# Optimization experiments

Measured on AMD Instinct MI355X. Metric: run time of the kernel, lower is better.

## Reference

```python
import jax, jax.numpy as jnp
import numpy as np

B, T, F, H = 256, 256, 128, 512


def setup_inputs() -> dict:
    key = jax.random.key(0)
    ks = jax.random.split(key, 16)
    values = jax.random.normal(ks[0], (B, T, F), dtype=jnp.float32)
    masks = (jax.random.uniform(ks[1], (B, T, F)) < 0.7).astype(jnp.float32)
    deltas = jax.random.uniform(ks[2], (B, T, F), dtype=jnp.float32) * 5.0
    empirical_mean = jax.random.normal(ks[3], (F,), dtype=jnp.float32)
    X_filledLOCF = jax.random.normal(ks[4], (B, T, F), dtype=jnp.float32)
    # TemporalDecay params: temp_decay_x is diag (F->F, diagonal weight), temp_decay_h is full (F->H)
    sF = 1.0 / np.sqrt(F)
    wx_diag = jax.random.uniform(ks[5], (F,), minval=-sF, maxval=sF, dtype=jnp.float32)
    bx = jax.random.uniform(ks[6], (F,), minval=-sF, maxval=sF, dtype=jnp.float32)
    Wh = jax.random.uniform(ks[7], (H, F), minval=-sF, maxval=sF, dtype=jnp.float32)
    bh = jax.random.uniform(ks[8], (H,), minval=-sF, maxval=sF, dtype=jnp.float32)
    # GRUCell params, torch layout: weight_ih [3H, 2F+H], weight_hh [3H, H], gate order r,z,n
    sH = 1.0 / np.sqrt(H)
    in_dim = 2 * F + H
    W_ih = jax.random.uniform(ks[9], (3 * H, in_dim), minval=-sH, maxval=sH, dtype=jnp.float32)
    W_hh = jax.random.uniform(ks[10], (3 * H, H), minval=-sH, maxval=sH, dtype=jnp.float32)
    b_ih = jax.random.uniform(ks[11], (3 * H,), minval=-sH, maxval=sH, dtype=jnp.float32)
    b_hh = jax.random.uniform(ks[12], (3 * H,), minval=-sH, maxval=sH, dtype=jnp.float32)
    return {"values": values, "masks": masks, "deltas": deltas,
            "empirical_mean": empirical_mean, "X_filledLOCF": X_filledLOCF,
            "wx_diag": wx_diag, "bx": bx, "Wh": Wh, "bh": bh,
            "W_ih": W_ih, "W_hh": W_hh, "b_ih": b_ih, "b_hh": b_hh}


def _grud_scan(values, masks, deltas, empirical_mean, X_filledLOCF,
               wx_diag, bx, Wh, bh, W_ih, W_hh, b_ih, b_hh):
    Hd = Wh.shape[0]
    h0 = jnp.zeros((values.shape[0], Hd), dtype=values.dtype)

    def step(h, xt):
        x, m, d, x_locf = xt  # each [B, F]
        gamma_h = jnp.exp(-jax.nn.relu(d @ Wh.T + bh))          # [B, H]
        gamma_x = jnp.exp(-jax.nn.relu(d * wx_diag + bx))       # [B, F] (diag TemporalDecay)
        h = h * gamma_h
        x_h = gamma_x * x_locf + (1.0 - gamma_x) * empirical_mean
        x_rep = m * x + (1.0 - m) * x_h
        inp = jnp.concatenate([x_rep, h, m], axis=1)            # [B, 2F+H]
        gi = inp @ W_ih.T + b_ih                                # [B, 3H]
        gh = h @ W_hh.T + b_hh                                  # [B, 3H]
        i_r, i_z, i_n = jnp.split(gi, 3, axis=1)
        h_r, h_z, h_n = jnp.split(gh, 3, axis=1)
        r = jax.nn.sigmoid(i_r + h_r)
        z = jax.nn.sigmoid(i_z + h_z)
        n = jnp.tanh(i_n + r * h_n)
        h_new = (1.0 - z) * n + z * h
        return h_new, h_new

    # time-major for scan: [T, B, F]
    xs = (values.transpose(1, 0, 2), masks.transpose(1, 0, 2),
          deltas.transpose(1, 0, 2), X_filledLOCF.transpose(1, 0, 2))
    h_last, hs = jax.lax.scan(step, h0, xs)
    return hs.transpose(1, 0, 2), h_last  # [B, T, H], [B, H]


def reference(values, masks, deltas, empirical_mean, X_filledLOCF,
              wx_diag, bx, Wh, bh, W_ih, W_hh, b_ih, b_hh):
    return _grud_scan(values, masks, deltas, empirical_mean, X_filledLOCF,
                      wx_diag, bx, Wh, bh, W_ih, W_hh, b_ih, b_hh)
```

## Files before the change

### kernel.cpp

```cpp
#include <hip/hip_runtime.h>
#include <math.h>

#define Bb 256
#define Tt 256
#define Ff 128
#define Hh 512
#define KTOT 768
#define NC 2048

typedef unsigned short u16;
typedef unsigned int   u32;
typedef unsigned long long u64;
typedef __attribute__((ext_vector_type(8))) short s8v;
typedef __attribute__((ext_vector_type(4))) float f4v;

#define OFF_GAMMA 0ull
#define OFF_XREP  (OFF_GAMMA + 67108864ull)
#define OFF_MBF   (OFF_XREP  + 16777216ull)
#define OFF_WFRAG (OFF_MBF   + 16777216ull)
#define OFF_BIASC (OFF_WFRAG + 3145728ull)
#define OFF_BAR   (OFF_BIASC + 8192ull)

__device__ __forceinline__ u16 f2b(float x) {
    u32 u = __float_as_uint(x);
    return (u16)((u + 0x7FFFu + ((u >> 16) & 1u)) >> 16);
}
__device__ __forceinline__ float b2f(u16 b) {
    return __uint_as_float(((u32)b) << 16);
}

__global__ __launch_bounds__(256) void k_zero(int* p, int n) {
    int i = blockIdx.x * 256 + threadIdx.x;
    if (i < n) p[i] = 0;
}

__device__ __forceinline__ float xrep_one(float x, float m, float d, float l,
                                          float w, float bb, float em) {
    float gx = expf(-fmaxf(d * w + bb, 0.f));
    float xh = gx * l + (1.f - gx) * em;
    return m * x + (1.f - m) * xh;
}

__global__ __launch_bounds__(256) void k_prep(const float* __restrict__ values,
                                              const float* __restrict__ masks,
                                              const float* __restrict__ deltas,
                                              const float* __restrict__ locf,
                                              const float* __restrict__ emean,
                                              const float* __restrict__ wx,
                                              const float* __restrict__ bxp,
                                              u16* __restrict__ xrep,
                                              u16* __restrict__ mbf) {
    int idx = blockIdx.x * 256 + threadIdx.x;
    int e = idx * 4;
    int f = e & 127;
    float4 xv = *(const float4*)&values[e];
    float4 mv = *(const float4*)&masks[e];
    float4 dv = *(const float4*)&deltas[e];
    float4 lv = *(const float4*)&locf[e];
    float4 wv = *(const float4*)&wx[f];
    float4 bv = *(const float4*)&bxp[f];
    float4 ev = *(const float4*)&emean[f];
    u16 o[4], mo[4];
    o[0] = f2b(xrep_one(xv.x, mv.x, dv.x, lv.x, wv.x, bv.x, ev.x));
    o[1] = f2b(xrep_one(xv.y, mv.y, dv.y, lv.y, wv.y, bv.y, ev.y));
    o[2] = f2b(xrep_one(xv.z, mv.z, dv.z, lv.z, wv.z, bv.z, ev.z));
    o[3] = f2b(xrep_one(xv.w, mv.w, dv.w, lv.w, wv.w, bv.w, ev.w));
    mo[0] = f2b(mv.x); mo[1] = f2b(mv.y); mo[2] = f2b(mv.z); mo[3] = f2b(mv.w);
    *(uint2*)&xrep[e] = *(uint2*)o;
    *(uint2*)&mbf[e]  = *(uint2*)mo;
}

__global__ __launch_bounds__(256) void k_wcomb(const float* __restrict__ W_ih,
                                               const float* __restrict__ W_hh,
                                               const float* __restrict__ b_ih,
                                               const float* __restrict__ b_hh,
                                               u16* __restrict__ wfrag,
                                               float* __restrict__ biasc) {
    int G = blockIdx.x * 256 + threadIdx.x;
    int lane = G & 63;
    int q = G >> 6;
    int ki = q % 24; q /= 24;
    int nt = q & 1;  q >>= 1;
    int wv = q & 3;  q >>= 2;
    int bx = q;
    int c = bx * 128 + wv * 32 + nt * 16 + (lane & 15);
    int kbase = ki * 32 + (lane >> 4) * 8;
    int g = c & 3, jH = c >> 2;
    u16 o[8];
#pragma unroll
    for (int j = 0; j < 8; ++j) {
        int k = kbase + j;
        float w;
        if (g < 3) {
            w = W_ih[(size_t)(g * Hh + jH) * KTOT + k];
            if (g < 2 && k >= Ff && k < Ff + Hh) w += W_hh[(size_t)(g * Hh + jH) * Hh + (k - Ff)];
        } else {
            w = (k >= Ff && k < Ff + Hh) ? W_hh[(size_t)(2 * Hh + jH) * Hh + (k - Ff)] : 0.f;
        }
        o[j] = f2b(w);
    }
    *(uint4*)&wfrag[(size_t)G * 8] = *(uint4*)o;
    if (ki == 0 && (lane >> 4) == 0) {
        float bv;
        if (g == 0)      bv = b_ih[jH] + b_hh[jH];
        else if (g == 1) bv = b_ih[Hh + jH] + b_hh[Hh + jH];
        else if (g == 2) bv = b_ih[2 * Hh + jH];
        else             bv = b_hh[2 * Hh + jH];
        biasc[c] = bv;
    }
}

__global__ __launch_bounds__(256) void k_gamma(const float* __restrict__ deltas,
                                               const float* __restrict__ Wh,
                                               const float* __restrict__ bh,
                                               u16* __restrict__ gamma) {
    __shared__ float A_s[64][68];
    __shared__ float B_s[64][68];
    int tid = threadIdx.x;
    int tx = tid & 15, ty = tid >> 4;
    int bt0 = blockIdx.x * 64;
    int c0  = blockIdx.y * 64;

    float acc[4][4];
#pragma unroll
    for (int i = 0; i < 4; ++i)
#pragma unroll
        for (int j = 0; j < 4; ++j) acc[i][j] = 0.f;

    for (int kc = 0; kc < 2; ++kc) {
#pragma unroll
        for (int s = 0; s < 4; ++s) {
            int v = tid + s * 256;
            int row = v >> 4, c4 = v & 15, kk = c4 * 4;
            int bt = bt0 + row;
            int b = bt & 255, tt = bt >> 8;
            float4 a = *(const float4*)&deltas[b * (Tt * Ff) + tt * Ff + kc * 64 + kk];
            *(float4*)&A_s[row][kk] = a;
        }
#pragma unroll
        for (int s = 0; s < 4; ++s) {
            int v = tid + s * 256;
            int col = v >> 4, c4 = v & 15, kk = c4 * 4;
            float4 w = *(const float4*)&Wh[(c0 + col) * Ff + kc * 64 + kk];
            *(float4*)&B_s[col][kk] = w;
        }
        __syncthreads();
#pragma unroll
        for (int kk = 0; kk < 64; kk += 4) {
            float4 a[4], b[4];
#pragma unroll
            for (int i = 0; i < 4; ++i) a[i] = *(const float4*)&A_s[4 * ty + i][kk];
#pragma unroll
            for (int j = 0; j < 4; ++j) b[j] = *(const float4*)&B_s[4 * tx + j][kk];
#pragma unroll
            for (int i = 0; i < 4; ++i)
#pragma unroll
                for (int j = 0; j < 4; ++j) {
                    acc[i][j] += a[i].x * b[j].x;
                    acc[i][j] += a[i].y * b[j].y;
                    acc[i][j] += a[i].z * b[j].z;
                    acc[i][j] += a[i].w * b[j].w;
                }
        }
        __syncthreads();
    }
#pragma unroll
    for (int i = 0; i < 4; ++i) {
        int bt = bt0 + 4 * ty + i;
        u16 o[4];
#pragma unroll
        for (int j = 0; j < 4; ++j) {
            int col = c0 + 4 * tx + j;
            float x = acc[i][j] + bh[col];
            o[j] = f2b(expf(-fmaxf(x, 0.f)));
        }
        *(uint2*)&gamma[(size_t)bt * Hh + c0 + 4 * tx] = *(uint2*)o;
    }
}

__global__ __launch_bounds__(256, 1) void k_scan(const u16* __restrict__ xrep,
                                                 const u16* __restrict__ mbf,
                                                 const u16* __restrict__ gamma,
                                                 const u16* __restrict__ wfrag,
                                                 const float* __restrict__ biasc,
                                                 int* __restrict__ bar,
                                                 float* __restrict__ hs,
                                                 float* __restrict__ hlast) {
    __shared__ u16  A_s[24 * 64 * 8];
    __shared__ float E_s[16][132];

    int tid = threadIdx.x;
    int lane = tid & 63, w = tid >> 6;

    int L = blockIdx.x + 16 * blockIdx.y;
    int by = (L & 7) + 8 * (L >> 7);
    int bx = (L >> 3) & 15;
    int r0 = by * 16;

    uint4 Bf[2][24];
    const uint4* wf4 = (const uint4*)wfrag;
#pragma unroll
    for (int nt = 0; nt < 2; ++nt)
#pragma unroll
        for (int ki = 0; ki < 24; ++ki)
            Bf[nt][ki] = wf4[(size_t)((((bx * 4 + w) * 2 + nt) * 24 + ki) * 64 + lane)];

    int srow = lane & 15;
    int koff = (lane >> 4) * 8;

    int bl = tid >> 4, jh0 = (tid & 15) * 2;
    int eb = r0 + bl;
    int JH0 = bx * 32 + jh0;
    float hreg0 = 0.f, hreg1 = 0.f;

    {
        int kb = w * 32 + koff;
        *(uint4*)&A_s[tid * 8] =
            *(const uint4*)&xrep[(size_t)(r0 + srow) * (Tt * Ff) + 0 * Ff + kb];
        *(uint4*)&A_s[(tid + 5 * 256) * 8] =
            *(const uint4*)&mbf[(size_t)(r0 + srow) * (Tt * Ff) + 0 * Ff + kb];
        uint4 z; z.x = 0; z.y = 0; z.z = 0; z.w = 0;
#pragma unroll
        for (int s = 1; s <= 4; ++s)
            *(uint4*)&A_s[(tid + s * 256) * 8] = z;
    }
    __syncthreads();

    for (int t = 0; t < Tt; ++t) {
        f4v acc0 = {0.f, 0.f, 0.f, 0.f};
        f4v acc1 = {0.f, 0.f, 0.f, 0.f};
#pragma unroll
        for (int ki = 0; ki < 24; ++ki) {
            s8v a = *(const s8v*)&A_s[(ki * 64 + lane) * 8];
            acc0 = __builtin_amdgcn_mfma_f32_16x16x32_bf16(a, __builtin_bit_cast(s8v, Bf[0][ki]), acc0, 0, 0, 0);
            acc1 = __builtin_amdgcn_mfma_f32_16x16x32_bf16(a, __builtin_bit_cast(s8v, Bf[1][ki]), acc1, 0, 0, 0);
        }

        {
            int colb = w * 32 + (lane & 15);
            int rq = (lane >> 4) * 4;
#pragma unroll
            for (int r = 0; r < 4; ++r) {
                E_s[rq + r][colb]      = acc0[r];
                E_s[rq + r][colb + 16] = acc1[r];
            }
        }
        __syncthreads();

        uint4 g4[4];
        if (t < Tt - 1) {
            int kb = w * 32 + koff;
            *(uint4*)&A_s[tid * 8] =
                *(const uint4*)&xrep[(size_t)(r0 + srow) * (Tt * Ff) + (t + 1) * Ff + kb];
            *(uint4*)&A_s[(tid + 5 * 256) * 8] =
                *(const uint4*)&mbf[(size_t)(r0 + srow) * (Tt * Ff) + (t + 1) * Ff + kb];
#pragma unroll
            for (int s = 1; s <= 4; ++s) {
                int kh = (s * 4 + w) * 32 + koff - 128;
                g4[s - 1] = *(const uint4*)&gamma[((size_t)(t + 1) * Bb + (r0 + srow)) * Hh + kh];
            }
        }

        float4 p0  = *(const float4*)&E_s[bl][jh0 * 4];
        float4 p1  = *(const float4*)&E_s[bl][jh0 * 4 + 4];
        float4 bi0 = *(const float4*)&biasc[JH0 * 4];
        float4 bi1 = *(const float4*)&biasc[JH0 * 4 + 4];
        float rg0 = 1.f / (1.f + expf(-(p0.x + bi0.x)));
        float zz0 = 1.f / (1.f + expf(-(p0.y + bi0.y)));
        float nn0 = tanhf(p0.z + bi0.z + rg0 * (p0.w + bi0.w));
        float hn0 = (1.f - zz0) * nn0 + zz0 * hreg0;
        float rg1 = 1.f / (1.f + expf(-(p1.x + bi1.x)));
        float zz1 = 1.f / (1.f + expf(-(p1.y + bi1.y)));
        float nn1 = tanhf(p1.z + bi1.z + rg1 * (p1.w + bi1.w));
        float hn1 = (1.f - zz1) * nn1 + zz1 * hreg1;

        union { float f[2]; u64 u; } pk;
        pk.f[0] = hn0; pk.f[1] = hn1;
        __hip_atomic_exchange((u64*)&hs[(size_t)eb * (Tt * Hh) + (size_t)t * Hh + JH0],
                              pk.u, __ATOMIC_RELAXED, __HIP_MEMORY_SCOPE_AGENT);

        if (t < Tt - 1) {
            u32 g = *(const u32*)&gamma[((size_t)(t + 1) * Bb + eb) * Hh + JH0];
            hreg0 = hn0 * b2f((u16)(g & 0xffffu));
            hreg1 = hn1 * b2f((u16)(g >> 16));

            asm volatile("s_waitcnt vmcnt(0)" ::: "memory");
            __syncthreads();
            if (tid == 0) {
                int* c = &bar[by * 32];
                __hip_atomic_fetch_add(c, 1, __ATOMIC_RELAXED, __HIP_MEMORY_SCOPE_AGENT);
                int target = 16 * (t + 1);
                int iters = 0;
                while (__hip_atomic_fetch_add(c, 0, __ATOMIC_RELAXED,
                                              __HIP_MEMORY_SCOPE_AGENT) < target) {
                    __builtin_amdgcn_s_sleep(1);
                    if (++iters > (1 << 22)) break;
                }
            }
            __syncthreads();

            float4 hb[8];
#pragma unroll
            for (int s = 1; s <= 4; ++s) {
                int kh = (s * 4 + w) * 32 + koff - 128;
                const float* hp = &hs[(size_t)(r0 + srow) * (Tt * Hh) + (size_t)t * Hh + kh];
                hb[2 * (s - 1)]     = *(const float4*)hp;
                hb[2 * (s - 1) + 1] = *(const float4*)(hp + 4);
            }
#pragma unroll
            for (int s = 1; s <= 4; ++s) {
                float4 h0 = hb[2 * (s - 1)];
                float4 h1 = hb[2 * (s - 1) + 1];
                u16 g8[8];
                *(uint4*)g8 = g4[s - 1];
                u16 o[8];
                o[0] = f2b(h0.x * b2f(g8[0])); o[1] = f2b(h0.y * b2f(g8[1]));
                o[2] = f2b(h0.z * b2f(g8[2])); o[3] = f2b(h0.w * b2f(g8[3]));
                o[4] = f2b(h1.x * b2f(g8[4])); o[5] = f2b(h1.y * b2f(g8[5]));
                o[6] = f2b(h1.z * b2f(g8[6])); o[7] = f2b(h1.w * b2f(g8[7]));
                *(uint4*)&A_s[(tid + s * 256) * 8] = *(uint4*)o;
            }
            __syncthreads();
        } else {
            float2 hn2; hn2.x = hn0; hn2.y = hn1;
            *(float2*)&hlast[eb * Hh + JH0] = hn2;
        }
    }
}

extern "C" void kernel_launch(void* const* d_in, const int* in_sizes, int n_in,
                              void* d_out, int out_size, void* d_ws, size_t ws_size,
                              hipStream_t stream) {
    const float* values = (const float*)d_in[0];
    const float* masks  = (const float*)d_in[1];
    const float* deltas = (const float*)d_in[2];
    const float* emean  = (const float*)d_in[3];
    const float* locf   = (const float*)d_in[4];
    const float* wx     = (const float*)d_in[5];
    const float* bxp    = (const float*)d_in[6];
    const float* Wh     = (const float*)d_in[7];
    const float* bh     = (const float*)d_in[8];
    const float* W_ih   = (const float*)d_in[9];
    const float* W_hh   = (const float*)d_in[10];
    const float* b_ih   = (const float*)d_in[11];
    const float* b_hh   = (const float*)d_in[12];

    char* wsb   = (char*)d_ws;
    u16*  gamma = (u16*)(wsb + OFF_GAMMA);
    u16*  xrep  = (u16*)(wsb + OFF_XREP);
    u16*  mbf   = (u16*)(wsb + OFF_MBF);
    u16*  wfrag = (u16*)(wsb + OFF_WFRAG);
    float* biasc = (float*)(wsb + OFF_BIASC);
    int*  bar   = (int*)(wsb + OFF_BAR);
    float* hs    = (float*)d_out;
    float* hlast = hs + (size_t)Bb * Tt * Hh;

    k_zero<<<2, 256, 0, stream>>>(bar, 512);
    k_prep<<<(Bb * Tt * Ff / 4) / 256, 256, 0, stream>>>(values, masks, deltas, locf,
                                                         emean, wx, bxp, xrep, mbf);
    k_gamma<<<dim3((Tt * Bb) / 64, Hh / 64), 256, 0, stream>>>(deltas, Wh, bh, gamma);
    k_wcomb<<<(NC * KTOT / 8) / 256, 256, 0, stream>>>(W_ih, W_hh, b_ih, b_hh, wfrag, biasc);

    k_scan<<<dim3(16, 16), 256, 0, stream>>>(xrep, mbf, gamma, wfrag, biasc,
                                             bar, hs, hlast);
}
```

Before: 1.924 ms.

## Split scan workgroup into eight waves each owning one MFMA column tile

The persistent scan kernel now runs 512 threads per block instead of 256. Each wave holds a single 16-column weight fragment set instead of two, and each thread computes one hidden unit's GRU update instead of two. The A-tile loading and h-refresh are redistributed across eight waves. The aim is to halve the serial MFMA chain and the per-thread register footprint on each step of the latency-bound recurrence, at the cost of more threads taking part in every block barrier.

New measurement: 1.685 ms. -12.4%, faster.

```diff
diff --git a/kernel.cpp b/kernel.cpp
--- a/kernel.cpp
+++ b/kernel.cpp
@@ -178,7 +178,7 @@
     }
 }
 
-__global__ __launch_bounds__(256, 1) void k_scan(const u16* __restrict__ xrep,
+__global__ __launch_bounds__(512, 2) void k_scan(const u16* __restrict__ xrep,
                                                  const u16* __restrict__ mbf,
                                                  const u16* __restrict__ gamma,
                                                  const u16* __restrict__ wfrag,
@@ -197,92 +197,90 @@
     int bx = (L >> 3) & 15;
     int r0 = by * 16;
 
-    uint4 Bf[2][24];
+    uint4 Bf[24];
     const uint4* wf4 = (const uint4*)wfrag;
 #pragma unroll
-    for (int nt = 0; nt < 2; ++nt)
-#pragma unroll
-        for (int ki = 0; ki < 24; ++ki)
-            Bf[nt][ki] = wf4[(size_t)((((bx * 4 + w) * 2 + nt) * 24 + ki) * 64 + lane)];
+    for (int ki = 0; ki < 24; ++ki)
+        Bf[ki] = wf4[(size_t)(((bx * 8 + w) * 24 + ki) * 64 + lane)];
 
     int srow = lane & 15;
     int koff = (lane >> 4) * 8;
 
-    int bl = tid >> 4, jh0 = (tid & 15) * 2;
+    int bl = tid >> 5, jh = tid & 31;
     int eb = r0 + bl;
-    int JH0 = bx * 32 + jh0;
-    float hreg0 = 0.f, hreg1 = 0.f;
+    int JH = bx * 32 + jh;
+    float4 bi = *(const float4*)&biasc[JH * 4];
+    float hreg = 0.f;
 
     {
-        int kb = w * 32 + koff;
-        *(uint4*)&A_s[tid * 8] =
-            *(const uint4*)&xrep[(size_t)(r0 + srow) * (Tt * Ff) + 0 * Ff + kb];
-        *(uint4*)&A_s[(tid + 5 * 256) * 8] =
-            *(const uint4*)&mbf[(size_t)(r0 + srow) * (Tt * Ff) + 0 * Ff + kb];
+        if (w < 4) {
+            int kb = w * 32 + koff;
+            *(uint4*)&A_s[tid * 8] =
+                *(const uint4*)&xrep[(size_t)(r0 + srow) * (Tt * Ff) + 0 * Ff + kb];
+        } else {
+            int kb = (w - 4) * 32 + koff;
+            *(uint4*)&A_s[(tid + 1024) * 8] =
+                *(const uint4*)&mbf[(size_t)(r0 + srow) * (Tt * Ff) + 0 * Ff + kb];
+        }
         uint4 z; z.x = 0; z.y = 0; z.z = 0; z.w = 0;
 #pragma unroll
-        for (int s = 1; s <= 4; ++s)
-            *(uint4*)&A_s[(tid + s * 256) * 8] = z;
+        for (int e = 0; e < 2; ++e) {
+            int ki = 4 + 8 * e + w;
+            *(uint4*)&A_s[(ki * 64 + lane) * 8] = z;
+        }
     }
     __syncthreads();
 
     for (int t = 0; t < Tt; ++t) {
-        f4v acc0 = {0.f, 0.f, 0.f, 0.f};
-        f4v acc1 = {0.f, 0.f, 0.f, 0.f};
+        f4v acc = {0.f, 0.f, 0.f, 0.f};
 #pragma unroll
         for (int ki = 0; ki < 24; ++ki) {
             s8v a = *(const s8v*)&A_s[(ki * 64 + lane) * 8];
-            acc0 = __builtin_amdgcn_mfma_f32_16x16x32_bf16(a, __builtin_bit_cast(s8v, Bf[0][ki]), acc0, 0, 0, 0);
-            acc1 = __builtin_amdgcn_mfma_f32_16x16x32_bf16(a, __builtin_bit_cast(s8v, Bf[1][ki]), acc1, 0, 0, 0);
+            acc = __builtin_amdgcn_mfma_f32_16x16x32_bf16(a, __builtin_bit_cast(s8v, Bf[ki]), acc, 0, 0, 0);
         }
 
         {
-            int colb = w * 32 + (lane & 15);
+            int colb = w * 16 + (lane & 15);
             int rq = (lane >> 4) * 4;
 #pragma unroll
-            for (int r = 0; r < 4; ++r) {
-                E_s[rq + r][colb]      = acc0[r];
-                E_s[rq + r][colb + 16] = acc1[r];
-            }
+            for (int r = 0; r < 4; ++r)
+                E_s[rq + r][colb] = acc[r];
         }
         __syncthreads();
 
-        uint4 g4[4];
+        uint4 g4[2];
+        u16 gdec = 0;
         if (t < Tt - 1) {
-            int kb = w * 32 + koff;
-            *(uint4*)&A_s[tid * 8] =
-                *(const uint4*)&xrep[(size_t)(r0 + srow) * (Tt * Ff) + (t + 1) * Ff + kb];
-            *(uint4*)&A_s[(tid + 5 * 256) * 8] =
-                *(const uint4*)&mbf[(size_t)(r0 + srow) * (Tt * Ff) + (t + 1) * Ff + kb];
-#pragma unroll
-            for (int s = 1; s <= 4; ++s) {
-                int kh = (s * 4 + w) * 32 + koff - 128;
-                g4[s - 1] = *(const uint4*)&gamma[((size_t)(t + 1) * Bb + (r0 + srow)) * Hh + kh];
-            }
-        }
-
-        float4 p0  = *(const float4*)&E_s[bl][jh0 * 4];
-        float4 p1  = *(const float4*)&E_s[bl][jh0 * 4 + 4];
-        float4 bi0 = *(const float4*)&biasc[JH0 * 4];
-        float4 bi1 = *(const float4*)&biasc[JH0 * 4 + 4];
-        float rg0 = 1.f / (1.f + expf(-(p0.x + bi0.x)));
-        float zz0 = 1.f / (1.f + expf(-(p0.y + bi0.y)));
-        float nn0 = tanhf(p0.z + bi0.z + rg0 * (p0.w + bi0.w));
-        float hn0 = (1.f - zz0) * nn0 + zz0 * hreg0;
-        float rg1 = 1.f / (1.f + expf(-(p1.x + bi1.x)));
-        float zz1 = 1.f / (1.f + expf(-(p1.y + bi1.y)));
-        float nn1 = tanhf(p1.z + bi1.z + rg1 * (p1.w + bi1.w));
-        float hn1 = (1.f - zz1) * nn1 + zz1 * hreg1;
-
-        union { float f[2]; u64 u; } pk;
-        pk.f[0] = hn0; pk.f[1] = hn1;
-        __hip_atomic_exchange((u64*)&hs[(size_t)eb * (Tt * Hh) + (size_t)t * Hh + JH0],
-                              pk.u, __ATOMIC_RELAXED, __HIP_MEMORY_SCOPE_AGENT);
+            if (w < 4) {
+                int kb = w * 32 + koff;
+                *(uint4*)&A_s[tid * 8] =
+                    *(const uint4*)&xrep[(size_t)(r0 + srow) * (Tt * Ff) + (t + 1) * Ff + kb];
+            } else {
+                int kb = (w - 4) * 32 + koff;
+                *(uint4*)&A_s[(tid + 1024) * 8] =
+                    *(const uint4*)&mbf[(size_t)(r0 + srow) * (Tt * Ff) + (t + 1) * Ff + kb];
+            }
+#pragma unroll
+            for (int e = 0; e < 2; ++e) {
+                int ki = 4 + 8 * e + w;
+                int kh = (ki - 4) * 32 + koff;
+                g4[e] = *(const uint4*)&gamma[((size_t)(t + 1) * Bb + (r0 + srow)) * Hh + kh];
+            }
+            gdec = gamma[((size_t)(t + 1) * Bb + eb) * Hh + JH];
+        }
+
+        float4 p = *(const float4*)&E_s[bl][jh * 4];
+        float rg = 1.f / (1.f + expf(-(p.x + bi.x)));
+        float zz = 1.f / (1.f + expf(-(p.y + bi.y)));
+        float nn = tanhf(p.z + bi.z + rg * (p.w + bi.w));
+        float hn = (1.f - zz) * nn + zz * hreg;
+
+        __hip_atomic_exchange((u32*)&hs[(size_t)eb * (Tt * Hh) + (size_t)t * Hh + JH],
+                              __float_as_uint(hn), __ATOMIC_RELAXED,
+                              __HIP_MEMORY_SCOPE_AGENT);
 
         if (t < Tt - 1) {
-            u32 g = *(const u32*)&gamma[((size_t)(t + 1) * Bb + eb) * Hh + JH0];
-            hreg0 = hn0 * b2f((u16)(g & 0xffffu));
-            hreg1 = hn1 * b2f((u16)(g >> 16));
+            hreg = hn * b2f(gdec);
 
             asm volatile("s_waitcnt vmcnt(0)" ::: "memory");
             __syncthreads();
@@ -299,31 +297,32 @@
             }
             __syncthreads();
 
-            float4 hb[8];
-#pragma unroll
-            for (int s = 1; s <= 4; ++s) {
-                int kh = (s * 4 + w) * 32 + koff - 128;
+            float4 hb[4];
+#pragma unroll
+            for (int e = 0; e < 2; ++e) {
+                int ki = 4 + 8 * e + w;
+                int kh = (ki - 4) * 32 + koff;
                 const float* hp = &hs[(size_t)(r0 + srow) * (Tt * Hh) + (size_t)t * Hh + kh];
-                hb[2 * (s - 1)]     = *(const float4*)hp;
-                hb[2 * (s - 1) + 1] = *(const float4*)(hp + 4);
-            }
-#pragma unroll
-            for (int s = 1; s <= 4; ++s) {
-                float4 h0 = hb[2 * (s - 1)];
-                float4 h1 = hb[2 * (s - 1) + 1];
+                hb[2 * e]     = *(const float4*)hp;
+                hb[2 * e + 1] = *(const float4*)(hp + 4);
+            }
+#pragma unroll
+            for (int e = 0; e < 2; ++e) {
+                int ki = 4 + 8 * e + w;
+                float4 h0 = hb[2 * e];
+                float4 h1 = hb[2 * e + 1];
                 u16 g8[8];
-                *(uint4*)g8 = g4[s - 1];
+                *(uint4*)g8 = g4[e];
                 u16 o[8];
                 o[0] = f2b(h0.x * b2f(g8[0])); o[1] = f2b(h0.y * b2f(g8[1]));
                 o[2] = f2b(h0.z * b2f(g8[2])); o[3] = f2b(h0.w * b2f(g8[3]));
                 o[4] = f2b(h1.x * b2f(g8[4])); o[5] = f2b(h1.y * b2f(g8[5]));
                 o[6] = f2b(h1.z * b2f(g8[6])); o[7] = f2b(h1.w * b2f(g8[7]));
-                *(uint4*)&A_s[(tid + s * 256) * 8] = *(uint4*)o;
+                *(uint4*)&A_s[(ki * 64 + lane) * 8] = *(uint4*)o;
             }
             __syncthreads();
         } else {
-            float2 hn2; hn2.x = hn0; hn2.y = hn1;
-            *(float2*)&hlast[eb * Hh + JH0] = hn2;
+            hlast[eb * Hh + JH] = hn;
         }
     }
 }
@@ -361,6 +360,6 @@
     k_gamma<<<dim3((Tt * Bb) / 64, Hh / 64), 256, 0, stream>>>(deltas, Wh, bh, gamma);
     k_wcomb<<<(NC * KTOT / 8) / 256, 256, 0, stream>>>(W_ih, W_hh, b_ih, b_hh, wfrag, biasc);
 
-    k_scan<<<dim3(16, 16), 256, 0, stream>>>(xrep, mbf, gamma, wfrag, biasc,
+    k_scan<<<dim3(16, 16), 512, 0, stream>>>(xrep, mbf, gamma, wfrag, biasc,
                                              bar, hs, hlast);
 }
```
